# Performance work log

Hardware: AMD Instinct MI355X
Metric: run time of the kernel (lower is better)

Reference implementation:

```python
import jax, jax.numpy as jnp
import numpy as np

N, IN, H, OUT, E = 4096, 128, 128, 2, 131072


def _hgnn(x, G, W, b):
    # HGNNConv (Feng et al.): X' = G @ (X W + b), G dense normalized [N,N]
    return G @ (x @ W + b)


def _mha(xin, Wqkv, bqkv, Wo, bo, nh):
    # torch.nn.MultiheadAttention, input (L, B, E), self-attention, eval mode
    L, B, Emb = xin.shape
    hd = Emb // nh
    qkv = xin @ Wqkv.T + bqkv                       # [L,B,3E]
    q, k, v = jnp.split(qkv, 3, axis=-1)
    def sh(t):
        return t.reshape(L, B, nh, hd).transpose(1, 2, 0, 3)  # [B,nh,L,hd]
    q, k, v = sh(q), sh(k), sh(v)
    att = jax.nn.softmax(jnp.einsum('bnld,bnmd->bnlm', q, k) / jnp.sqrt(jnp.float32(hd)), axis=-1)
    o = jnp.einsum('bnlm,bnmd->bnld', att, v).transpose(2, 0, 1, 3).reshape(L, B, Emb)
    return o @ Wo.T + bo


def setup_inputs() -> dict:
    key = jax.random.key(0)
    ks = jax.random.split(key, 40)
    d = {}
    d['x'] = jax.random.normal(ks[0], (N, IN), jnp.float32)
    # dense normalized hypergraph propagation matrices (rand, scaled ~1/N so rows sum ~1)
    d['hg_1hop'] = jax.random.uniform(ks[1], (N, N), jnp.float32) * (2.0 / N)
    d['hg_3hop'] = jax.random.uniform(ks[2], (N, N), jnp.float32) * (2.0 / N)
    d['edge_indices'] = jax.random.randint(ks[3], (2, E), 0, N).astype(jnp.int32)
    d['new_idb'] = jax.random.permutation(ks[4], N).astype(jnp.int32)
    d['lam'] = jax.random.uniform(ks[5], (1,), jnp.float32)
    d['beta'] = jnp.asarray(0.3, jnp.float32)
    i = 6
    def w(shape, s):
        nonlocal i
        out = jax.random.normal(ks[i], shape, jnp.float32) * s
        i += 1
        return out
    sw = 1.0 / np.sqrt(H)
    d['W1'] = w((IN, H), 1.0 / np.sqrt(IN)); d['b1'] = w((H,), 0.01)
    for nm in ['W2', 'W3', 'W1h', 'W3h', 'W2m', 'W3m']:
        d[nm] = w((H, H), sw); d['b' + nm[1:]] = w((H,), 0.01)
    for tag in ['mix', 'fus']:
        d['Wqkv_' + tag] = w((3 * H, H), sw); d['bqkv_' + tag] = w((3 * H,), 0.01)
        d['Wo_' + tag] = w((H, H), sw); d['bo_' + tag] = w((H,), 0.01)
    d['Wc'] = w((2 * H, OUT), 1.0 / np.sqrt(2 * H)); d['bc'] = w((OUT,), 0.01)
    return d


def reference(x, hg_1hop, hg_3hop, edge_indices, new_idb, lam, beta,
              W1, b1, W2, b2, W3, b3, W1h, b1h, W3h, b3h, W2m, b2m, W3m, b3m,
              Wqkv_mix, bqkv_mix, Wo_mix, bo_mix,
              Wqkv_fus, bqkv_fus, Wo_fus, bo_fus, Wc, bc):
    # eval mode: dropout = identity
    h1 = jax.nn.relu(_hgnn(x, hg_1hop, W1, b1))
    h2 = jax.nn.relu(_hgnn(h1, hg_1hop, W2, b2) + h1)
    h3_c1 = jax.nn.relu(_hgnn(h2, hg_1hop, W3, b3) + h2)

    # shuffle_hypergraph: permute nodes of the dense incidence-derived matrix
    hg1_b = hg_1hop[new_idb][:, new_idb]
    hg3_b = hg_3hop[new_idb][:, new_idb]
    l = lam[0]
    # mixup_hidden: manifold mixup of propagated features with permuted graph/features
    h1_mix_1hop = l * _hgnn(h1, hg_1hop, W1h, b1h) + (1.0 - l) * _hgnn(h1[new_idb], hg1_b, W1h, b1h)
    h1_mix_3hop = l * _hgnn(h1, hg_3hop, W3h, b3h) + (1.0 - l) * _hgnn(h1[new_idb], hg3_b, W3h, b3h)

    h1_stack = jnp.stack([h1_mix_1hop, h1_mix_3hop], axis=0)     # [2,N,H]
    h1_mix = _mha(h1_stack, Wqkv_mix, bqkv_mix, Wo_mix, bo_mix, 2).mean(axis=0)
    h2_mix = jax.nn.relu(_hgnn(h1_mix, hg_1hop, W2m, b2m) + h1_mix)
    h3_c2 = jax.nn.relu(_hgnn(h2_mix, hg_1hop, W3m, b3m) + h2_mix) * beta

    h3_stack = jnp.stack([h3_c1, h3_c2], axis=0)                 # [2,N,H]
    h3 = _mha(h3_stack, Wqkv_fus, bqkv_fus, Wo_fus, bo_fus, 4).mean(axis=0)

    edge_emb = jnp.concatenate([h3[edge_indices[0]], h3[edge_indices[1]]], axis=1)  # [E,2H]
    edge_pred = edge_emb @ Wc + bc
    return edge_pred, h3
```

## Files before the change

### kernel.cpp

```cpp
#include <hip/hip_runtime.h>
#include <math.h>

typedef unsigned short u16;
typedef short s8v __attribute__((ext_vector_type(8)));
typedef float f4v __attribute__((ext_vector_type(4)));

__device__ inline float b2f(u16 u) {
    union { unsigned int i; float f; } v; v.i = ((unsigned int)u) << 16; return v.f;
}
__device__ inline u16 f2b(float f) {
    unsigned int x = __float_as_uint(f);
    return (u16)((x + 0x7fffu + ((x >> 16) & 1u)) >> 16);
}
__device__ inline float ldf(const void* p, size_t i, int f32) {
    return f32 ? ((const float*)p)[i] : b2f(((const u16*)p)[i]);
}
__device__ inline s8v load8(const void* p, size_t idx, int f32) {
    if (f32) {
        const float* f = (const float*)p + idx;
        float4 a = *(const float4*)(f);
        float4 b = *(const float4*)(f + 4);
        s8v r;
        r[0] = (short)f2b(a.x); r[1] = (short)f2b(a.y);
        r[2] = (short)f2b(a.z); r[3] = (short)f2b(a.w);
        r[4] = (short)f2b(b.x); r[5] = (short)f2b(b.y);
        r[6] = (short)f2b(b.z); r[7] = (short)f2b(b.w);
        return r;
    }
    return *(const s8v*)((const u16*)p + idx);
}

__global__ __launch_bounds__(256) void convert_g1(const void* __restrict__ G1,
                                                  u16* __restrict__ G1b,
                                                  int* __restrict__ dflag,
                                                  int doCopy) {
    __shared__ int s_flag;
    const int tid = threadIdx.x, bid = blockIdx.x;
    if (tid == 0) s_flag = 0;
    __syncthreads();
    {
        int bad = 0;
        for (int i = tid; i < 2048; i += 256) {
            float v = b2f(((const u16*)G1)[i]);
            if (!(fabsf(v) <= 1e-3f)) bad = 1;
        }
        if (bad) atomicOr(&s_flag, 1);
    }
    __syncthreads();
    const int f32 = s_flag;
    if (bid == 0 && tid == 0) *dflag = f32;
    if (!doCopy) return;
    const int gid = bid * 256 + tid;
    for (size_t c = (size_t)gid; c < 2097152; c += 262144)
        *(s8v*)(G1b + c * 8) = load8(G1, c * 8, f32);
}

struct BigJob { const void* G; const u16* Zt; float* part; int gF32; };
struct BigP { BigJob j[3]; };

__global__ __launch_bounds__(256) void big_v2(BigP P, int kLen,
                                              const int* __restrict__ dflag) {
    __shared__ u16 At[64 * 72];
    __shared__ u16 Bt[128 * 72];
    const BigJob jb = P.j[blockIdx.z];
    const int f32 = jb.gF32 ? *dflag : 0;
    const int tid = threadIdx.x;
    const int rowBase = blockIdx.x * 64;
    const int kChunk = blockIdx.y * kLen;
    const int nIter = kLen >> 6;
    const int w = tid >> 6, lane = tid & 63;
    const int wm = w & 1, wn = w >> 1;
    const int l15 = lane & 15, quad = lane >> 4;
    const int rA0 = tid >> 3, rA1 = 32 + (tid >> 3), kb = tid & 7;
    const u16* Zt = jb.Zt;

    f4v acc[2][4] = {};
    s8v a0, a1, b0, b1, b2, b3;
    {
        const int kBase = kChunk;
        a0 = load8(jb.G, (size_t)(rowBase + rA0) * 4096 + kBase + kb * 8, f32);
        a1 = load8(jb.G, (size_t)(rowBase + rA1) * 4096 + kBase + kb * 8, f32);
        b0 = *(const s8v*)(Zt + (size_t)(rA0) * 4096 + kBase + kb * 8);
        b1 = *(const s8v*)(Zt + (size_t)(rA0 + 32) * 4096 + kBase + kb * 8);
        b2 = *(const s8v*)(Zt + (size_t)(rA0 + 64) * 4096 + kBase + kb * 8);
        b3 = *(const s8v*)(Zt + (size_t)(rA0 + 96) * 4096 + kBase + kb * 8);
    }
    for (int it = 0; it < nIter; ++it) {
        __syncthreads();
        *(s8v*)(At + rA0 * 72 + kb * 8) = a0;
        *(s8v*)(At + rA1 * 72 + kb * 8) = a1;
        *(s8v*)(Bt + rA0 * 72 + kb * 8) = b0;
        *(s8v*)(Bt + (rA0 + 32) * 72 + kb * 8) = b1;
        *(s8v*)(Bt + (rA0 + 64) * 72 + kb * 8) = b2;
        *(s8v*)(Bt + (rA0 + 96) * 72 + kb * 8) = b3;
        __syncthreads();
        if (it + 1 < nIter) {
            const int kBase = kChunk + (it + 1) * 64;
            a0 = load8(jb.G, (size_t)(rowBase + rA0) * 4096 + kBase + kb * 8, f32);
            a1 = load8(jb.G, (size_t)(rowBase + rA1) * 4096 + kBase + kb * 8, f32);
            b0 = *(const s8v*)(Zt + (size_t)(rA0) * 4096 + kBase + kb * 8);
            b1 = *(const s8v*)(Zt + (size_t)(rA0 + 32) * 4096 + kBase + kb * 8);
            b2 = *(const s8v*)(Zt + (size_t)(rA0 + 64) * 4096 + kBase + kb * 8);
            b3 = *(const s8v*)(Zt + (size_t)(rA0 + 96) * 4096 + kBase + kb * 8);
        }
#pragma unroll
        for (int ks = 0; ks < 2; ++ks) {
            s8v af[2], bf[4];
            const int ko = (ks * 4 + quad) * 8;
#pragma unroll
            for (int mi = 0; mi < 2; ++mi)
                af[mi] = *(const s8v*)(At + (wm * 32 + mi * 16 + l15) * 72 + ko);
#pragma unroll
            for (int ni = 0; ni < 4; ++ni)
                bf[ni] = *(const s8v*)(Bt + (wn * 64 + ni * 16 + l15) * 72 + ko);
#pragma unroll
            for (int mi = 0; mi < 2; ++mi)
#pragma unroll
                for (int ni = 0; ni < 4; ++ni)
                    acc[mi][ni] = __builtin_amdgcn_mfma_f32_16x16x32_bf16(
                        af[mi], bf[ni], acc[mi][ni], 0, 0, 0);
        }
    }
    float* pbase = jb.part + (size_t)blockIdx.y * 524288;
#pragma unroll
    for (int mi = 0; mi < 2; ++mi)
#pragma unroll
        for (int ni = 0; ni < 4; ++ni) {
            int row = rowBase + wm * 32 + mi * 16 + quad * 4;
            int col = wn * 64 + ni * 16 + l15;
#pragma unroll
            for (int r = 0; r < 4; ++r)
                pbase[(size_t)(row + r) * 128 + col] = acc[mi][ni][r];
        }
}

struct EpiJob { const float* part; const u16* res; u16* out; int mode; };
struct EpiP { EpiJob j[3]; const void* betap; };

__global__ __launch_bounds__(256) void epi_v2(EpiP P, int S,
                                              const int* __restrict__ dflag) {
    const EpiJob J = P.j[blockIdx.z];
    int i = (blockIdx.x * 256 + threadIdx.x) * 4;
    f4v t = {};
    for (int s = 0; s < S; ++s)
        t += *(const f4v*)(J.part + (size_t)s * 524288 + i);
    float bscale = (J.mode == 2) ? ldf(P.betap, 0, *dflag) : 1.0f;
    u16 o[4];
#pragma unroll
    for (int k = 0; k < 4; ++k) {
        float v = t[k];
        if (J.mode == 1 || J.mode == 2) v += b2f(J.res[i + k]);
        if (J.mode <= 2) v = fmaxf(v, 0.0f);
        if (J.mode == 2) v *= bscale;
        o[k] = f2b(v);
    }
    *(ushort4*)(J.out + i) = make_ushort4(o[0], o[1], o[2], o[3]);
}

struct FeatJob { const void* A; const void* W; const void* bias; void* out;
                 u16* mir; size_t outOfs; int wLayout; int outMode; int aMode; };
struct FeatP { FeatJob j[3]; const u16* Ph1; const u16* Ph3;
               const int* perm; const void* lam; };

__global__ __launch_bounds__(256) void feat_v2(FeatP P, int M, int NcTotal,
                                               const int* __restrict__ dflag) {
    __shared__ char smemf[52224];
    u16* Wt = (u16*)smemf;
    u16* At = (u16*)(smemf + 34816);
    u16* Tt = (u16*)smemf;
    const FeatJob J = P.j[blockIdx.z];
    const int f32 = *dflag;
    const int tid = threadIdx.x;
    const int rowBase = blockIdx.x * 64;
    const int colBase = blockIdx.y * 128;

    if (J.wLayout == 1) {
#pragma unroll
        for (int i = 0; i < 8; ++i) {
            int c = i * 256 + tid;
            int n = c >> 4, kb = c & 15;
            *(s8v*)(Wt + n * 136 + kb * 8) =
                load8(J.W, (size_t)(colBase + n) * 128 + kb * 8, f32);
        }
    } else {
#pragma unroll
        for (int i = 0; i < 64; ++i) {
            int idx = i * 256 + tid;
            int k = idx >> 7, n = idx & 127;
            Wt[n * 136 + k] = f2b(ldf(J.W, (size_t)k * NcTotal + colBase + n, f32));
        }
    }
    if (J.aMode == 2) {
        float l = ldf(P.lam, 0, f32);
#pragma unroll
        for (int i = 0; i < 4; ++i) {
            int c = i * 256 + tid;
            int r = c >> 4, kb = c & 15;
            int grow = rowBase + r;
            const u16* src = (grow < 4096) ? P.Ph1 : P.Ph3;
            int n = grow & 4095;
            int pn = P.perm[n];
            s8v va = *(const s8v*)(src + (size_t)n * 128 + kb * 8);
            s8v vb = *(const s8v*)(src + (size_t)pn * 128 + kb * 8);
            s8v r8;
#pragma unroll
            for (int q = 0; q < 8; ++q)
                r8[q] = (short)f2b(l * b2f((u16)va[q]) + (1.0f - l) * b2f((u16)vb[q]));
            *(s8v*)(At + r * 136 + kb * 8) = r8;
        }
    } else {
        const int aF32 = (J.aMode == 1) ? f32 : 0;
#pragma unroll
        for (int i = 0; i < 4; ++i) {
            int c = i * 256 + tid;
            int r = c >> 4, kb = c & 15;
            *(s8v*)(At + r * 136 + kb * 8) =
                load8(J.A, (size_t)(rowBase + r) * 128 + kb * 8, aF32);
        }
    }
    __syncthreads();

    const int w = tid >> 6, lane = tid & 63, l15 = lane & 15, quad = lane >> 4;
    f4v acc[8] = {};
#pragma unroll
    for (int ks = 0; ks < 4; ++ks) {
        int k = ks * 32 + quad * 8;
        s8v a = *(const s8v*)(At + (w * 16 + l15) * 136 + k);
#pragma unroll
        for (int ni = 0; ni < 8; ++ni) {
            s8v b = *(const s8v*)(Wt + (ni * 16 + l15) * 136 + k);
            acc[ni] = __builtin_amdgcn_mfma_f32_16x16x32_bf16(a, b, acc[ni], 0, 0, 0);
        }
    }

    if (J.outMode == 0) {
#pragma unroll
        for (int ni = 0; ni < 8; ++ni) {
            int n = colBase + ni * 16 + l15;
            float bv = ldf(J.bias, n, f32);
#pragma unroll
            for (int r = 0; r < 4; ++r) {
                int row = rowBase + w * 16 + quad * 4 + r;
                ((u16*)J.out)[(size_t)row * NcTotal + n] = f2b(acc[ni][r] + bv);
            }
        }
    } else if (J.outMode == 2) {
#pragma unroll
        for (int ni = 0; ni < 8; ++ni) {
            int n = colBase + ni * 16 + l15;
            float bv = ldf(J.bias, n, f32);
#pragma unroll
            for (int r = 0; r < 4; ++r) {
                int row = rowBase + w * 16 + quad * 4 + r;
                size_t idx = (size_t)row * NcTotal + n;
                float v = acc[ni][r] + bv;
                u16 vb = f2b(v);
                J.mir[idx] = vb;
                if (f32) ((float*)J.out)[J.outOfs + idx] = v;
                else     ((u16*)J.out)[J.outOfs + idx] = vb;
            }
        }
    } else {
        __syncthreads();
#pragma unroll
        for (int ni = 0; ni < 8; ++ni) {
            int n = ni * 16 + l15;
            float bv = ldf(J.bias, colBase + n, f32);
#pragma unroll
            for (int r = 0; r < 4; ++r)
                Tt[n * 72 + (w * 16 + quad * 4 + r)] = f2b(acc[ni][r] + bv);
        }
        __syncthreads();
#pragma unroll
        for (int i = 0; i < 4; ++i) {
            int c = i * 256 + tid;
            int h = c >> 3, nb = c & 7;
            s8v v = *(const s8v*)(Tt + h * 72 + nb * 8);
            *(s8v*)((u16*)J.out + (size_t)(colBase + h) * M + rowBase + nb * 8) = v;
        }
    }
}

__global__ __launch_bounds__(256) void attn_kernel(const u16* __restrict__ qkv,
                                                   u16* __restrict__ obar, int nh) {
    int wid = threadIdx.x >> 6, lane = threadIdx.x & 63;
    int n = blockIdx.x * 4 + wid;
    const u16* r0 = qkv + (size_t)n * 384;
    const u16* r1 = qkv + (size_t)(4096 + n) * 384;
    int hd = 128 / nh;
    float scale = 1.0f / sqrtf((float)hd);
    float ov[2];
#pragma unroll
    for (int e = 0; e < 2; ++e) {
        int h = e * 64 + lane;
        float q0 = b2f(r0[h]),       q1 = b2f(r1[h]);
        float k0 = b2f(r0[128 + h]), k1 = b2f(r1[128 + h]);
        float v0 = b2f(r0[256 + h]), v1 = b2f(r1[256 + h]);
        float s00 = q0 * k0, s01 = q0 * k1, s10 = q1 * k0, s11 = q1 * k1;
        for (int off = hd >> 1; off; off >>= 1) {
            s00 += __shfl_xor(s00, off);
            s01 += __shfl_xor(s01, off);
            s10 += __shfl_xor(s10, off);
            s11 += __shfl_xor(s11, off);
        }
        s00 *= scale; s01 *= scale; s10 *= scale; s11 *= scale;
        float m0 = fmaxf(s00, s01), m1 = fmaxf(s10, s11);
        float e00 = expf(s00 - m0), e01 = expf(s01 - m0);
        float e10 = expf(s10 - m1), e11 = expf(s11 - m1);
        float a00 = e00 / (e00 + e01), a01 = e01 / (e00 + e01);
        float a10 = e10 / (e10 + e11), a11 = e11 / (e10 + e11);
        ov[e] = 0.5f * ((a00 * v0 + a01 * v1) + (a10 * v0 + a11 * v1));
    }
    obar[(size_t)n * 128 + lane] = f2b(ov[0]);
    obar[(size_t)n * 128 + 64 + lane] = f2b(ov[1]);
}

__global__ __launch_bounds__(256) void edge_kernel(const u16* __restrict__ h3,
                                                   const int* __restrict__ eidx,
                                                   const void* __restrict__ Wc,
                                                   const void* __restrict__ bc,
                                                   void* __restrict__ out,
                                                   const int* __restrict__ dflag) {
    __shared__ float w0[256], w1[256];
    const int f32 = *dflag;
    int t = threadIdx.x;
    w0[t] = ldf(Wc, (size_t)t * 2, f32);
    w1[t] = ldf(Wc, (size_t)t * 2 + 1, f32);
    __syncthreads();
    int e = blockIdx.x * 256 + t;
    float a0 = ldf(bc, 0, f32), a1 = ldf(bc, 1, f32);
#pragma unroll
    for (int p = 0; p < 2; ++p) {
        int node = eidx[p * 131072 + e];
        const s8v* row = (const s8v*)(h3 + (size_t)node * 128);
#pragma unroll
        for (int cch = 0; cch < 16; ++cch) {
            s8v d = row[cch];
#pragma unroll
            for (int j = 0; j < 8; ++j) {
                float f = b2f((u16)d[j]);
                int k = p * 128 + cch * 8 + j;
                a0 += f * w0[k];
                a1 += f * w1[k];
            }
        }
    }
    if (f32) {
        ((float*)out)[(size_t)e * 2] = a0;
        ((float*)out)[(size_t)e * 2 + 1] = a1;
    } else {
        ((u16*)out)[(size_t)e * 2] = f2b(a0);
        ((u16*)out)[(size_t)e * 2 + 1] = f2b(a1);
    }
}

extern "C" void kernel_launch(void* const* d_in, const int* in_sizes, int n_in,
                              void* d_out, int out_size, void* d_ws, size_t ws_size,
                              hipStream_t stream) {
    const void* x    = d_in[0];
    const void* G1   = d_in[1];
    const void* G3   = d_in[2];
    const int* eidx = (const int*)d_in[3];
    const int* perm = (const int*)d_in[4];
    const void* lam  = d_in[5];
    const void* beta = d_in[6];
    const void* W1 = d_in[7],  *b1 = d_in[8];
    const void* W2 = d_in[9],  *b2 = d_in[10];
    const void* W3 = d_in[11], *b3 = d_in[12];
    const void* W1h = d_in[13], *b1h = d_in[14];
    const void* W3h = d_in[15], *b3h = d_in[16];
    const void* W2m = d_in[17], *b2m = d_in[18];
    const void* W3m = d_in[19], *b3m = d_in[20];
    const void* Wqkv_mix = d_in[21], *bqkv_mix = d_in[22];
    const void* Wo_mix   = d_in[23], *bo_mix   = d_in[24];
    const void* Wqkv_fus = d_in[25], *bqkv_fus = d_in[26];
    const void* Wo_fus   = d_in[27], *bo_fus   = d_in[28];
    const void* Wc = d_in[29], *bc = d_in[30];

    const size_t MB = 1ull << 20;
    char* base = (char*)d_ws;
    const bool tier1 = ws_size >= 100 * MB;
    const int Ssing = tier1 ? 16 : 4;
    const int Sbat  = tier1 ? 8 : 2;
    u16* G1b = (u16*)base;
    char* pool = base + (tier1 ? 32 : 0) * MB;
    const size_t poolSz = (size_t)(tier1 ? 48 : 12) * MB;
    char* persist = pool + poolSz;
    u16* Zt0   = (u16*)(persist + 0 * MB);
    u16* Zt1   = (u16*)(persist + 1 * MB);
    u16* Zt2   = (u16*)(persist + 2 * MB);
    u16* Zt3   = (u16*)(persist + 3 * MB);
    u16* h1    = (u16*)(persist + 4 * MB);
    u16* h2    = (u16*)(persist + 5 * MB);
    u16* h3c1  = (u16*)(persist + 6 * MB);
    u16* h1mix = (u16*)(persist + 7 * MB);
    u16* h2mix = (u16*)(persist + 8 * MB);
    u16* h3c2  = (u16*)(persist + 9 * MB);
    u16* Ph1   = (u16*)(persist + 10 * MB);
    u16* Ph3   = (u16*)(persist + 11 * MB);
    u16* mir   = (u16*)(persist + 12 * MB);
    u16* qkv   = (u16*)(persist + 13 * MB);
    int* dflag = (int*)(persist + 19 * MB);
    float* part0 = (float*)pool;
    float* part1 = (float*)(pool + (size_t)Sbat * 2 * MB);
    float* part2 = (float*)(pool + (size_t)2 * Sbat * 2 * MB);

    const void* G1use = tier1 ? (const void*)G1b : G1;
    const int g1F32 = tier1 ? 0 : 1;

    auto featN = [&](FeatP& FP, int nz, int M, int Nc) {
        feat_v2<<<dim3(M / 64, Nc / 128, nz), 256, 0, stream>>>(FP, M, Nc, dflag);
    };
    auto feat1 = [&](const void* A, const void* W, const void* b, void* o,
                     int M, int Nc, int wl, int om, int am,
                     u16* mr = nullptr, size_t ofs = 0) {
        FeatP FP = {};
        FP.j[0] = { A, W, b, o, mr, ofs, wl, om, am };
        FP.Ph1 = Ph1; FP.Ph3 = Ph3; FP.perm = perm; FP.lam = lam;
        featN(FP, 1, M, Nc);
    };
    auto big1 = [&](const void* Gm, int gF32, const u16* Zt, float* part) {
        BigP BP = {};
        BP.j[0] = { Gm, Zt, part, gF32 };
        big_v2<<<dim3(64, Ssing, 1), 256, 0, stream>>>(BP, 4096 / Ssing, dflag);
    };
    auto epi1 = [&](const float* part, const u16* res, u16* o, int mode) {
        EpiP EP = {};
        EP.j[0] = { part, res, o, mode };
        EP.betap = beta;
        epi_v2<<<dim3(512, 1, 1), 256, 0, stream>>>(EP, Ssing, dflag);
    };

    convert_g1<<<1024, 256, 0, stream>>>(G1, G1b, dflag, tier1 ? 1 : 0);
    feat1(x, W1, b1, Zt0, 4096, 128, 0, 1, 1);
    big1(G1use, g1F32, Zt0, part0);
    epi1(part0, nullptr, h1, 0);
    {
        FeatP FP = {};
        FP.j[0] = { h1, W2,  b2,  Zt1, nullptr, 0, 0, 1, 0 };
        FP.j[1] = { h1, W1h, b1h, Zt2, nullptr, 0, 0, 1, 0 };
        FP.j[2] = { h1, W3h, b3h, Zt3, nullptr, 0, 0, 1, 0 };
        FP.Ph1 = Ph1; FP.Ph3 = Ph3; FP.perm = perm; FP.lam = lam;
        featN(FP, 3, 4096, 128);
    }
    {
        BigP BP = {};
        BP.j[0] = { G1use, Zt1, part0, g1F32 };
        BP.j[1] = { G1use, Zt2, part1, g1F32 };
        BP.j[2] = { G3,    Zt3, part2, 1 };
        big_v2<<<dim3(64, Sbat, 3), 256, 0, stream>>>(BP, 4096 / Sbat, dflag);
    }
    {
        EpiP EP = {};
        EP.j[0] = { part0, h1, h2, 1 };
        EP.j[1] = { part1, nullptr, Ph1, 3 };
        EP.j[2] = { part2, nullptr, Ph3, 3 };
        EP.betap = beta;
        epi_v2<<<dim3(512, 1, 3), 256, 0, stream>>>(EP, Sbat, dflag);
    }
    feat1(h2, W3, b3, Zt0, 4096, 128, 0, 1, 0);
    big1(G1use, g1F32, Zt0, part0);
    feat1(nullptr, Wqkv_mix, bqkv_mix, qkv, 8192, 384, 1, 0, 2);
    epi1(part0, h2, h3c1, 1);
    attn_kernel<<<1024, 256, 0, stream>>>(qkv, (u16*)Zt0, 2);
    feat1(Zt0, Wo_mix, bo_mix, h1mix, 4096, 128, 1, 0, 0);
    feat1(h1mix, W2m, b2m, Zt1, 4096, 128, 0, 1, 0);
    big1(G1use, g1F32, Zt1, part0);
    epi1(part0, h1mix, h2mix, 1);
    feat1(h2mix, W3m, b3m, Zt1, 4096, 128, 0, 1, 0);
    big1(G1use, g1F32, Zt1, part0);
    epi1(part0, h2mix, h3c2, 2);
    {
        FeatP FP = {};
        FP.j[0] = { h3c1, Wqkv_fus, bqkv_fus, qkv, nullptr, 0, 1, 0, 0 };
        FP.j[1] = { h3c2, Wqkv_fus, bqkv_fus, qkv + (size_t)4096 * 384, nullptr, 0, 1, 0, 0 };
        FP.Ph1 = Ph1; FP.Ph3 = Ph3; FP.perm = perm; FP.lam = lam;
        featN(FP, 2, 4096, 384);
    }
    attn_kernel<<<1024, 256, 0, stream>>>(qkv, (u16*)Zt0, 4);
    feat1(Zt0, Wo_fus, bo_fus, d_out, 4096, 128, 1, 2, 0, mir, (size_t)131072 * 2);
    edge_kernel<<<512, 256, 0, stream>>>(mir, eidx, Wc, bc, d_out, dflag);
}
```

Baseline: 540.1 us.

## Shrink big GEMM row tile and load A fragments directly from global

The dense G@Z kernel now uses 32-row tiles with 128 blocks in x and loads each wave's A fragments straight from global memory into registers, dropping the A shared-memory tile and its LDS round trip. The split-K factor is fixed at 4 for both single and batched launches (previously 16/8 or 4/2 depending on workspace), which cuts partial-sum traffic in the epilogue. In exchange, per-block B tile reuse halves, each Z tile is loaded by twice as many blocks, and the A global loads become less coalesced (16 rows by 8 elements per wave).

```diff
diff --git a/kernel.cpp b/kernel.cpp
--- a/kernel.cpp
+++ b/kernel.cpp
@@ -58,80 +58,66 @@
 struct BigJob { const void* G; const u16* Zt; float* part; int gF32; };
 struct BigP { BigJob j[3]; };
 
-__global__ __launch_bounds__(256) void big_v2(BigP P, int kLen,
+__global__ __launch_bounds__(256) void big_v3(BigP P, int kLen,
                                               const int* __restrict__ dflag) {
-    __shared__ u16 At[64 * 72];
     __shared__ u16 Bt[128 * 72];
     const BigJob jb = P.j[blockIdx.z];
     const int f32 = jb.gF32 ? *dflag : 0;
     const int tid = threadIdx.x;
-    const int rowBase = blockIdx.x * 64;
+    const int rowBase = blockIdx.x * 32;
     const int kChunk = blockIdx.y * kLen;
     const int nIter = kLen >> 6;
     const int w = tid >> 6, lane = tid & 63;
     const int wm = w & 1, wn = w >> 1;
     const int l15 = lane & 15, quad = lane >> 4;
-    const int rA0 = tid >> 3, rA1 = 32 + (tid >> 3), kb = tid & 7;
+    const int bn = tid >> 3, bkb = tid & 7;
+    const size_t arow = (size_t)(rowBase + wm * 16 + l15) * 4096;
     const u16* Zt = jb.Zt;
 
-    f4v acc[2][4] = {};
-    s8v a0, a1, b0, b1, b2, b3;
-    {
-        const int kBase = kChunk;
-        a0 = load8(jb.G, (size_t)(rowBase + rA0) * 4096 + kBase + kb * 8, f32);
-        a1 = load8(jb.G, (size_t)(rowBase + rA1) * 4096 + kBase + kb * 8, f32);
-        b0 = *(const s8v*)(Zt + (size_t)(rA0) * 4096 + kBase + kb * 8);
-        b1 = *(const s8v*)(Zt + (size_t)(rA0 + 32) * 4096 + kBase + kb * 8);
-        b2 = *(const s8v*)(Zt + (size_t)(rA0 + 64) * 4096 + kBase + kb * 8);
-        b3 = *(const s8v*)(Zt + (size_t)(rA0 + 96) * 4096 + kBase + kb * 8);
+    f4v acc[4] = {};
+    s8v bpre[4], apre[2];
+    {
+        const int kB = kChunk;
+#pragma unroll
+        for (int i = 0; i < 4; ++i)
+            bpre[i] = *(const s8v*)(Zt + (size_t)(bn + i * 32) * 4096 + kB + bkb * 8);
+        apre[0] = load8(jb.G, arow + kB + quad * 8, f32);
+        apre[1] = load8(jb.G, arow + kB + 32 + quad * 8, f32);
     }
     for (int it = 0; it < nIter; ++it) {
         __syncthreads();
-        *(s8v*)(At + rA0 * 72 + kb * 8) = a0;
-        *(s8v*)(At + rA1 * 72 + kb * 8) = a1;
-        *(s8v*)(Bt + rA0 * 72 + kb * 8) = b0;
-        *(s8v*)(Bt + (rA0 + 32) * 72 + kb * 8) = b1;
-        *(s8v*)(Bt + (rA0 + 64) * 72 + kb * 8) = b2;
-        *(s8v*)(Bt + (rA0 + 96) * 72 + kb * 8) = b3;
+#pragma unroll
+        for (int i = 0; i < 4; ++i)
+            *(s8v*)(Bt + (bn + i * 32) * 72 + bkb * 8) = bpre[i];
         __syncthreads();
+        s8v a0 = apre[0], a1 = apre[1];
         if (it + 1 < nIter) {
-            const int kBase = kChunk + (it + 1) * 64;
-            a0 = load8(jb.G, (size_t)(rowBase + rA0) * 4096 + kBase + kb * 8, f32);
-            a1 = load8(jb.G, (size_t)(rowBase + rA1) * 4096 + kBase + kb * 8, f32);
-            b0 = *(const s8v*)(Zt + (size_t)(rA0) * 4096 + kBase + kb * 8);
-            b1 = *(const s8v*)(Zt + (size_t)(rA0 + 32) * 4096 + kBase + kb * 8);
-            b2 = *(const s8v*)(Zt + (size_t)(rA0 + 64) * 4096 + kBase + kb * 8);
-            b3 = *(const s8v*)(Zt + (size_t)(rA0 + 96) * 4096 + kBase + kb * 8);
+            const int kB = kChunk + (it + 1) * 64;
+#pragma unroll
+            for (int i = 0; i < 4; ++i)
+                bpre[i] = *(const s8v*)(Zt + (size_t)(bn + i * 32) * 4096 + kB + bkb * 8);
+            apre[0] = load8(jb.G, arow + kB + quad * 8, f32);
+            apre[1] = load8(jb.G, arow + kB + 32 + quad * 8, f32);
         }
 #pragma unroll
         for (int ks = 0; ks < 2; ++ks) {
-            s8v af[2], bf[4];
-            const int ko = (ks * 4 + quad) * 8;
-#pragma unroll
-            for (int mi = 0; mi < 2; ++mi)
-                af[mi] = *(const s8v*)(At + (wm * 32 + mi * 16 + l15) * 72 + ko);
-#pragma unroll
-            for (int ni = 0; ni < 4; ++ni)
-                bf[ni] = *(const s8v*)(Bt + (wn * 64 + ni * 16 + l15) * 72 + ko);
-#pragma unroll
-            for (int mi = 0; mi < 2; ++mi)
-#pragma unroll
-                for (int ni = 0; ni < 4; ++ni)
-                    acc[mi][ni] = __builtin_amdgcn_mfma_f32_16x16x32_bf16(
-                        af[mi], bf[ni], acc[mi][ni], 0, 0, 0);
+            s8v a = ks ? a1 : a0;
+#pragma unroll
+            for (int ni = 0; ni < 4; ++ni) {
+                s8v b = *(const s8v*)(Bt + (wn * 64 + ni * 16 + l15) * 72 + (ks * 4 + quad) * 8);
+                acc[ni] = __builtin_amdgcn_mfma_f32_16x16x32_bf16(a, b, acc[ni], 0, 0, 0);
+            }
         }
     }
     float* pbase = jb.part + (size_t)blockIdx.y * 524288;
-#pragma unroll
-    for (int mi = 0; mi < 2; ++mi)
-#pragma unroll
-        for (int ni = 0; ni < 4; ++ni) {
-            int row = rowBase + wm * 32 + mi * 16 + quad * 4;
-            int col = wn * 64 + ni * 16 + l15;
-#pragma unroll
-            for (int r = 0; r < 4; ++r)
-                pbase[(size_t)(row + r) * 128 + col] = acc[mi][ni][r];
-        }
+    const int row = rowBase + wm * 16 + quad * 4;
+#pragma unroll
+    for (int ni = 0; ni < 4; ++ni) {
+        int col = wn * 64 + ni * 16 + l15;
+#pragma unroll
+        for (int r = 0; r < 4; ++r)
+            pbase[(size_t)(row + r) * 128 + col] = acc[ni][r];
+    }
 }
 
 struct EpiJob { const float* part; const u16* res; u16* out; int mode; };
@@ -380,12 +366,10 @@
     const size_t MB = 1ull << 20;
     char* base = (char*)d_ws;
     const bool tier1 = ws_size >= 100 * MB;
-    const int Ssing = tier1 ? 16 : 4;
-    const int Sbat  = tier1 ? 8 : 2;
+    const int S = 4;
     u16* G1b = (u16*)base;
     char* pool = base + (tier1 ? 32 : 0) * MB;
-    const size_t poolSz = (size_t)(tier1 ? 48 : 12) * MB;
-    char* persist = pool + poolSz;
+    char* persist = pool + 24 * MB;
     u16* Zt0   = (u16*)(persist + 0 * MB);
     u16* Zt1   = (u16*)(persist + 1 * MB);
     u16* Zt2   = (u16*)(persist + 2 * MB);
@@ -402,8 +386,8 @@
     u16* qkv   = (u16*)(persist + 13 * MB);
     int* dflag = (int*)(persist + 19 * MB);
     float* part0 = (float*)pool;
-    float* part1 = (float*)(pool + (size_t)Sbat * 2 * MB);
-    float* part2 = (float*)(pool + (size_t)2 * Sbat * 2 * MB);
+    float* part1 = (float*)(pool + 8 * MB);
+    float* part2 = (float*)(pool + 16 * MB);
 
     const void* G1use = tier1 ? (const void*)G1b : G1;
     const int g1F32 = tier1 ? 0 : 1;
@@ -422,13 +406,13 @@
     auto big1 = [&](const void* Gm, int gF32, const u16* Zt, float* part) {
         BigP BP = {};
         BP.j[0] = { Gm, Zt, part, gF32 };
-        big_v2<<<dim3(64, Ssing, 1), 256, 0, stream>>>(BP, 4096 / Ssing, dflag);
+        big_v3<<<dim3(128, S, 1), 256, 0, stream>>>(BP, 4096 / S, dflag);
     };
     auto epi1 = [&](const float* part, const u16* res, u16* o, int mode) {
         EpiP EP = {};
         EP.j[0] = { part, res, o, mode };
         EP.betap = beta;
-        epi_v2<<<dim3(512, 1, 1), 256, 0, stream>>>(EP, Ssing, dflag);
+        epi_v2<<<dim3(512, 1, 1), 256, 0, stream>>>(EP, S, dflag);
     };
 
     convert_g1<<<1024, 256, 0, stream>>>(G1, G1b, dflag, tier1 ? 1 : 0);
@@ -448,7 +432,7 @@
         BP.j[0] = { G1use, Zt1, part0, g1F32 };
         BP.j[1] = { G1use, Zt2, part1, g1F32 };
         BP.j[2] = { G3,    Zt3, part2, 1 };
-        big_v2<<<dim3(64, Sbat, 3), 256, 0, stream>>>(BP, 4096 / Sbat, dflag);
+        big_v3<<<dim3(128, S, 3), 256, 0, stream>>>(BP, 4096 / S, dflag);
     }
     {
         EpiP EP = {};
@@ -456,7 +440,7 @@
         EP.j[1] = { part1, nullptr, Ph1, 3 };
         EP.j[2] = { part2, nullptr, Ph3, 3 };
         EP.betap = beta;
-        epi_v2<<<dim3(512, 1, 3), 256, 0, stream>>>(EP, Sbat, dflag);
+        epi_v2<<<dim3(512, 1, 3), 256, 0, stream>>>(EP, S, dflag);
     }
     feat1(h2, W3, b3, Zt0, 4096, 128, 0, 1, 0);
     big1(G1use, g1F32, Zt0, part0);
```

Measured after the change: 564.3 us. +4.5%, slower.
